# Kernel optimization log

Hardware: AMD Instinct MI355X
Metric: run time of the kernel (lower is better)

Reference implementation:

```python
import jax, jax.numpy as jnp
import numpy as np

N, IN, H, OUT, C = 1024, 64, 64, 64, 32
EPS = 1e-5   # SAKELayer.epsilon
INF = 1e5    # SAKELayer.inf


def _w(key, i, o, scale=1.0):
    return jax.random.normal(key, (i, o), jnp.float32) * (scale / np.sqrt(i))


def setup_inputs() -> dict:
    key = jax.random.key(0)
    ks = jax.random.split(key, 16)
    return dict(
        h=jax.random.normal(ks[0], (N, IN), jnp.float32),
        x=jax.random.normal(ks[1], (N, 3), jnp.float32),
        # edge model (ConcatenationFilter): Linear(2*IN+1,H), SiLU, Linear(H,H)
        ew1=_w(ks[2], 2 * IN + 1, H), eb1=jnp.zeros((H,), jnp.float32),
        ew2=_w(ks[3], H, H), eb2=jnp.zeros((H,), jnp.float32),
        # node_mlp: Linear(2H+IN,H), SiLU, Linear(H,OUT)
        nw1=_w(ks[4], 2 * H + IN, H), nb1=jnp.zeros((H,), jnp.float32),
        nw2=_w(ks[5], H, OUT), nb2=jnp.zeros((OUT,), jnp.float32),
        # coordinate_mlp: Linear(H,H), SiLU, Linear(H,1,bias=False) xavier gain 1e-3
        cw1=_w(ks[6], H, H), cb1=jnp.zeros((H,), jnp.float32),
        cw2=_w(ks[7], H, 1, scale=1e-3),
        # semantic_attention_mlp: Linear(H,1), LeakyReLU
        aw=_w(ks[8], H, 1), ab=jnp.zeros((1,), jnp.float32),
        # coefficients_mlp: Linear(H,H), SiLU, Linear(H,C)
        fw1=_w(ks[9], H, H), fb1=jnp.zeros((H,), jnp.float32),
        fw2=_w(ks[10], H, C), fb2=jnp.zeros((C,), jnp.float32),
        # post_norm_mlp: Linear(C,H), SiLU, Linear(H,H)
        pw1=_w(ks[11], C, H), pb1=jnp.zeros((H,), jnp.float32),
        pw2=_w(ks[12], H, H), pb2=jnp.zeros((H,), jnp.float32),
        log_gamma=jnp.array(0.0, jnp.float32),
    )


def reference(h, x, ew1, eb1, ew2, eb2, nw1, nb1, nw2, nb2, cw1, cb1, cw2,
              aw, ab, fw1, fb1, fw2, fb2, pw1, pb1, pw2, pb2, log_gamma):
    n, d_in = h.shape
    silu = jax.nn.silu
    eye = jnp.eye(n, dtype=h.dtype)[:, :, None]                    # [n,n,1]

    x_minus_xt = x[:, None, :] - x[None, :, :]                     # [n,n,3]
    norm = jnp.sqrt(jnp.sum(x_minus_xt ** 2, -1, keepdims=True) + EPS)  # [n,n,1]

    h_cat_ht = jnp.concatenate(
        [jnp.broadcast_to(h[:, None, :], (n, n, d_in)),
         jnp.broadcast_to(h[None, :, :], (n, n, d_in))], -1)       # [n,n,2*IN]

    # edge model: MLP over concat(features, distance)
    e_in = jnp.concatenate([h_cat_ht, norm], -1)                   # [n,n,2*IN+1]
    h_e = silu(e_in @ ew1 + eb1) @ ew2 + eb2                       # [n,n,H]

    # euclidean attention over neighbors j (diag masked by +INF distance)
    att_e = jax.nn.softmax(-(norm + INF * eye) * jnp.exp(log_gamma), axis=1)
    # semantic attention
    att_s = jax.nn.softmax(jax.nn.leaky_relu(h_e @ aw + ab) - INF * eye, axis=1)
    comb = att_e * att_s
    comb = comb / (jnp.sum(comb, axis=1, keepdims=True) + EPS)     # [n,n,1]
    h_e_att = h_e * comb                                           # [n,n,H]

    # spatial attention: equivariant coefficient combinations
    coeff = silu(h_e_att @ fw1 + fb1) @ fw2 + fb2                  # [n,n,C]
    dirs = x_minus_xt / (norm + 1.0)                               # [n,n,3]
    combos = jnp.einsum('ijc,ijd->icd', coeff, dirs) / n           # mean over j -> [n,C,3]
    h_comb = silu(jnp.sum(combos ** 2, -1) @ pw1 + pb1) @ pw2 + pb2  # [n,H]

    # node update
    h_agg = jnp.sum(h_e_att, axis=1)                               # [n,H]
    node_in = jnp.concatenate([h, h_agg, h_comb], -1)              # [n,2H+IN]
    h_out = h + (silu(node_in @ nw1 + nb1) @ nw2 + nb2)            # residual

    # equivariant coordinate update
    phi = silu(h_e @ cw1 + cb1) @ cw2                              # [n,n,1]
    x_out = x + jnp.mean(x_minus_xt * phi, axis=1)                 # [n,3]
    return h_out, x_out
```

## Files before the change

kernel.cpp:

```cpp
#include <hip/hip_runtime.h>
#include <hip/hip_bf16.h>

#define NN 1024
#define JT 128
#define LSTR 72
#define EPSV 1e-5f
#define BIGINF 1e5f

typedef __attribute__((ext_vector_type(8))) short short8;
typedef __attribute__((ext_vector_type(4))) short short4v;
typedef __attribute__((ext_vector_type(4))) float f32x4;

__device__ __forceinline__ float siluf(float v) {
    return v * __builtin_amdgcn_rcpf(1.0f + __expf(-v));
}
__device__ __forceinline__ float pnorm(float dx, float dy, float dz) {
    return sqrtf(dx * dx + dy * dy + dz * dz + EPSV);
}
__device__ __forceinline__ float wsum(float v) {
#pragma unroll
    for (int off = 32; off > 0; off >>= 1) v += __shfl_xor(v, off, 64);
    return v;
}
__device__ __forceinline__ float red16(float v) {
    v += __shfl_xor(v, 1, 64); v += __shfl_xor(v, 2, 64);
    v += __shfl_xor(v, 4, 64); v += __shfl_xor(v, 8, 64);
    return v;
}
__device__ __forceinline__ float redquad(float v) {
    v += __shfl_xor(v, 16, 64); v += __shfl_xor(v, 32, 64);
    return v;
}
__device__ __forceinline__ short f2bs(float v) {
    __hip_bfloat16 b = __float2bfloat16(v);
    return *reinterpret_cast<short*>(&b);
}
__device__ __forceinline__ short f2bt(float v) {
    return (short)(__float_as_uint(v) >> 16);
}

__global__ void kA(const float* __restrict__ h, const float* __restrict__ ew1,
                   const float* __restrict__ eb1, const float* __restrict__ ew2,
                   const float* __restrict__ cw1, const float* __restrict__ fw1,
                   const float* __restrict__ fw2, const float* __restrict__ aw,
                   const float* __restrict__ ab, const float* __restrict__ eb2,
                   float* __restrict__ HA, float* __restrict__ HB,
                   float* __restrict__ HBT, short* __restrict__ ew2T,
                   short* __restrict__ cw1T, short* __restrict__ fw1T,
                   short* __restrict__ fw2T, float* __restrict__ wsv,
                   float* __restrict__ svb) {
    const int b = blockIdx.x;
    const int o = threadIdx.x;
    if (b < NN) {
        const int i = b;
        float hv = h[i * 64 + o];
        float a = 0.f, bb = eb1[o];
#pragma unroll
        for (int k = 0; k < 64; k++) {
            float hk = __shfl(hv, k, 64);
            a += hk * ew1[k * 64 + o];
            bb += hk * ew1[(64 + k) * 64 + o];
        }
        HA[i * 64 + o] = a;
        HB[i * 64 + o] = bb;
        HBT[o * NN + i] = bb;
    } else if (b < NN + 64) {
        const int r = b - NN;
        ew2T[r * 64 + o] = f2bs(ew2[o * 64 + r]);
        cw1T[r * 64 + o] = f2bs(cw1[o * 64 + r]);
        fw1T[r * 64 + o] = f2bs(fw1[o * 64 + r]);
        if (r < 32) fw2T[r * 64 + o] = f2bs(fw2[o * 32 + r]);
    } else {
        float s = 0.f;
#pragma unroll
        for (int q = 0; q < 64; q++) s += ew2[o * 64 + q] * aw[q];
        wsv[o] = s;
        float e = wsum(eb2[o] * aw[o]);
        if (o == 0) svb[0] = e + ab[0];
    }
}

__global__ __launch_bounds__(256) void kBn(
    const float* __restrict__ x, const float* __restrict__ ew1,
    const float* __restrict__ HA, const float* __restrict__ HBT,
    const float* __restrict__ wsv, const float* __restrict__ svb,
    const float* __restrict__ lg, float* __restrict__ ls,
    float* __restrict__ rowm, float* __restrict__ rowd) {
    const int i = blockIdx.x;
    const int t = threadIdx.x;
    const float* HAi = HA + i * 64;
    const float* w1 = ew1 + 128 * 64;
    const float gamma = __expf(lg[0]);
    const float svb0 = svb[0];
    const float xi0 = x[i * 3 + 0], xi1 = x[i * 3 + 1], xi2 = x[i * 3 + 2];

    float4 xa = ((const float4*)x)[3 * t + 0];
    float4 xb = ((const float4*)x)[3 * t + 1];
    float4 xc = ((const float4*)x)[3 * t + 2];
    float nrm[4], le[4], lv[4];
    {
        float dx0 = xi0 - xa.x, dy0 = xi1 - xa.y, dz0 = xi2 - xa.z;
        float dx1 = xi0 - xa.w, dy1 = xi1 - xb.x, dz1 = xi2 - xb.y;
        float dx2 = xi0 - xb.z, dy2 = xi1 - xb.w, dz2 = xi2 - xc.x;
        float dx3 = xi0 - xc.y, dy3 = xi1 - xc.z, dz3 = xi2 - xc.w;
        nrm[0] = pnorm(dx0, dy0, dz0);
        nrm[1] = pnorm(dx1, dy1, dz1);
        nrm[2] = pnorm(dx2, dy2, dz2);
        nrm[3] = pnorm(dx3, dy3, dz3);
    }
    float d0 = 0.f, d1 = 0.f, d2 = 0.f, d3 = 0.f;
#pragma unroll 8
    for (int k = 0; k < 64; k++) {
        float4 hb = *(const float4*)&HBT[k * NN + 4 * t];
        float hk = HAi[k], w1k = w1[k], wv = wsv[k];
        d0 += siluf(hk + hb.x + nrm[0] * w1k) * wv;
        d1 += siluf(hk + hb.y + nrm[1] * w1k) * wv;
        d2 += siluf(hk + hb.z + nrm[2] * w1k) * wv;
        d3 += siluf(hk + hb.w + nrm[3] * w1k) * wv;
    }
    float me = -3.0e38f, ms = -3.0e38f;
    float4 svo;
    {
        float dd[4] = {d0, d1, d2, d3};
#pragma unroll
        for (int m = 0; m < 4; m++) {
            int j = 4 * t + m;
            float sv = dd[m] + svb0;
            sv = sv >= 0.f ? sv : 0.01f * sv;
            if (j == i) sv -= BIGINF;
            lv[m] = sv;
            le[m] = -(nrm[m] + (j == i ? BIGINF : 0.f)) * gamma;
            me = fmaxf(me, le[m]);
            ms = fmaxf(ms, lv[m]);
        }
        svo.x = lv[0]; svo.y = lv[1]; svo.z = lv[2]; svo.w = lv[3];
    }
    *(float4*)&ls[(size_t)i * NN + 4 * t] = svo;

    __shared__ float sm[4], ss[4], s1[4], s2[4], s3[4];
#pragma unroll
    for (int off = 32; off > 0; off >>= 1) {
        me = fmaxf(me, __shfl_xor(me, off, 64));
        ms = fmaxf(ms, __shfl_xor(ms, off, 64));
    }
    const int w = t >> 6;
    if ((t & 63) == 0) { sm[w] = me; ss[w] = ms; }
    __syncthreads();
    me = fmaxf(fmaxf(sm[0], sm[1]), fmaxf(sm[2], sm[3]));
    ms = fmaxf(fmaxf(ss[0], ss[1]), fmaxf(ss[2], ss[3]));
    float Se = 0.f, Ss = 0.f, Sq = 0.f;
#pragma unroll
    for (int m = 0; m < 4; m++) {
        float ee = __expf(le[m] - me);
        float es = __expf(lv[m] - ms);
        Se += ee; Ss += es; Sq += ee * es;
    }
    Se = wsum(Se); Ss = wsum(Ss); Sq = wsum(Sq);
    if ((t & 63) == 0) { s1[w] = Se; s2[w] = Ss; s3[w] = Sq; }
    __syncthreads();
    if (t == 0) {
        rowm[i] = me + ms;
        rowd[i] = (s3[0] + s3[1] + s3[2] + s3[3]) +
                  EPSV * (s1[0] + s1[1] + s1[2] + s1[3]) * (s2[0] + s2[1] + s2[2] + s2[3]);
    }
}

__device__ __forceinline__ void stageW(const short* __restrict__ g, short* s,
                                       int tid, int rows) {
    for (int c = tid; c < rows * 16; c += 512) {
        int r = c >> 4, q = c & 15;
        *(short4v*)&s[r * LSTR + q * 4] = *(const short4v*)&g[r * 64 + q * 4];
    }
}

__global__ __launch_bounds__(512) void kD(
    const float* __restrict__ x, const float* __restrict__ ew1,
    const float* __restrict__ eb2, const float* __restrict__ cb1,
    const float* __restrict__ cw2, const float* __restrict__ fb1,
    const float* __restrict__ fb2, const float* __restrict__ lg,
    const float* __restrict__ HA, const float* __restrict__ HB,
    const short* __restrict__ ew2T, const short* __restrict__ cw1T,
    const short* __restrict__ fw1T, const short* __restrict__ fw2T,
    const float* __restrict__ ls, const float* __restrict__ rowm,
    const float* __restrict__ rowd, float* __restrict__ hagg,
    float* __restrict__ combos, float* __restrict__ xupd) {
    __shared__ __align__(16) short sWe[64 * LSTR];
    __shared__ __align__(16) short sWc[64 * LSTR];
    __shared__ __align__(16) short sWf[64 * LSTR];
    __shared__ __align__(16) short sW2[32 * LSTR];
    __shared__ __align__(16) short sScr[8][16 * LSTR];
    __shared__ float sHag[64], sCombos[96], sXupd[3];

    const int tid = threadIdx.x;
    const int i = blockIdx.x;
    const int lane = tid & 63, w = tid >> 6;
    const int col = lane & 15, quad = lane >> 4;

    stageW(ew2T, sWe, tid, 64);
    stageW(cw1T, sWc, tid, 64);
    stageW(fw1T, sWf, tid, 64);
    stageW(fw2T, sW2, tid, 32);
    if (tid < 64) sHag[tid] = 0.f;
    else if (tid < 160) sCombos[tid - 64] = 0.f;
    else if (tid < 163) sXupd[tid - 160] = 0.f;

    short* scr = sScr[w];
    const float gamma = __expf(lg[0]);

    float w1r[2][8], har[2][8];
#pragma unroll
    for (int kb = 0; kb < 2; kb++)
#pragma unroll
        for (int t = 0; t < 8; t++) {
            w1r[kb][t] = ew1[128 * 64 + kb * 32 + quad * 8 + t];
            har[kb][t] = HA[i * 64 + kb * 32 + quad * 8 + t];
        }
    float eb[4], cbv[4], cwv[4], fbv[4];
#pragma unroll
    for (int nb = 0; nb < 4; nb++) {
        eb[nb] = eb2[nb * 16 + col];
        cbv[nb] = cb1[nb * 16 + col];
        cwv[nb] = cw2[nb * 16 + col];
        fbv[nb] = fb1[nb * 16 + col];
    }
    float fb2v[2] = {fb2[col], fb2[16 + col]};
    const float rm = rowm[i];
    const float invd = 1.0f / rowd[i];
    const float xi0 = x[i * 3 + 0], xi1 = x[i * 3 + 1], xi2 = x[i * 3 + 2];
    const float* lsi = ls + (size_t)i * NN;
    __syncthreads();

#pragma unroll 1
    for (int jt = 0; jt < 8; jt++) {
        const int jrow = jt * JT + w * 16 + col;
        float dxv = xi0 - x[jrow * 3 + 0];
        float dyv = xi1 - x[jrow * 3 + 1];
        float dzv = xi2 - x[jrow * 3 + 2];
        float nrmv = pnorm(dxv, dyv, dzv);
        float inv1 = __builtin_amdgcn_rcpf(nrmv + 1.0f);
        float fxv = dxv * inv1, fyv = dyv * inv1, fzv = dzv * inv1;
        float le = -(nrmv + (jrow == i ? BIGINF : 0.f)) * gamma;
        float combv = __expf(le + lsi[jrow] - rm) * invd;

        short8 afr[2];
#pragma unroll
        for (int kb = 0; kb < 2; kb++) {
            const float* hb = &HB[jrow * 64 + kb * 32 + quad * 8];
#pragma unroll
            for (int t = 0; t < 8; t++)
                afr[kb][t] = f2bt(siluf(har[kb][t] + hb[t] + nrmv * w1r[kb][t]));
        }
        f32x4 acc[4] = {{0.f, 0.f, 0.f, 0.f}, {0.f, 0.f, 0.f, 0.f},
                        {0.f, 0.f, 0.f, 0.f}, {0.f, 0.f, 0.f, 0.f}};
#pragma unroll
        for (int kb = 0; kb < 2; kb++) {
#pragma unroll
            for (int nb = 0; nb < 4; nb++) {
                short8 b = *(const short8*)&sWe[(nb * 16 + col) * LSTR + kb * 32 + quad * 8];
                acc[nb] = __builtin_amdgcn_mfma_f32_16x16x32_bf16(afr[kb], b, acc[nb], 0, 0, 0);
            }
        }
        {
            float hv[4][4], cmb[4];
#pragma unroll
            for (int reg = 0; reg < 4; reg++) cmb[reg] = __shfl(combv, quad * 4 + reg, 64);
#pragma unroll
            for (int reg = 0; reg < 4; reg++) {
#pragma unroll
                for (int nb = 0; nb < 4; nb++) {
                    hv[nb][reg] = acc[nb][reg] + eb[nb];
                    scr[(quad * 4 + reg) * LSTR + nb * 16 + col] = f2bt(hv[nb][reg]);
                }
            }
#pragma unroll
            for (int nb = 0; nb < 4; nb++) {
                float v = 0.f;
#pragma unroll
                for (int reg = 0; reg < 4; reg++) v += hv[nb][reg] * cmb[reg];
                v = redquad(v);
                if (quad == 0) atomicAdd(&sHag[nb * 16 + col], v);
            }
        }
        short8 a0 = *(const short8*)&scr[col * LSTR + quad * 8];
        short8 a1 = *(const short8*)&scr[col * LSTR + 32 + quad * 8];

        {
            f32x4 p[4] = {{0.f, 0.f, 0.f, 0.f}, {0.f, 0.f, 0.f, 0.f},
                          {0.f, 0.f, 0.f, 0.f}, {0.f, 0.f, 0.f, 0.f}};
#pragma unroll
            for (int nb = 0; nb < 4; nb++) {
                short8 b0 = *(const short8*)&sWc[(nb * 16 + col) * LSTR + quad * 8];
                short8 b1 = *(const short8*)&sWc[(nb * 16 + col) * LSTR + 32 + quad * 8];
                p[nb] = __builtin_amdgcn_mfma_f32_16x16x32_bf16(a0, b0, p[nb], 0, 0, 0);
                p[nb] = __builtin_amdgcn_mfma_f32_16x16x32_bf16(a1, b1, p[nb], 0, 0, 0);
            }
            float xa0 = 0.f, xa1 = 0.f, xa2 = 0.f;
#pragma unroll
            for (int reg = 0; reg < 4; reg++) {
                float ph = 0.f;
#pragma unroll
                for (int nb = 0; nb < 4; nb++) ph += siluf(p[nb][reg] + cbv[nb]) * cwv[nb];
                ph = red16(ph);
                float tdx = __shfl(dxv, quad * 4 + reg, 64);
                float tdy = __shfl(dyv, quad * 4 + reg, 64);
                float tdz = __shfl(dzv, quad * 4 + reg, 64);
                if (col == 0) { xa0 += ph * tdx; xa1 += ph * tdy; xa2 += ph * tdz; }
            }
            xa0 = wsum(xa0); xa1 = wsum(xa1); xa2 = wsum(xa2);
            if (lane == 0) {
                atomicAdd(&sXupd[0], xa0);
                atomicAdd(&sXupd[1], xa1);
                atomicAdd(&sXupd[2], xa2);
            }
        }

        {
            f32x4 vacc[4] = {{0.f, 0.f, 0.f, 0.f}, {0.f, 0.f, 0.f, 0.f},
                             {0.f, 0.f, 0.f, 0.f}, {0.f, 0.f, 0.f, 0.f}};
#pragma unroll
            for (int nb = 0; nb < 4; nb++) {
                short8 b0 = *(const short8*)&sWf[(nb * 16 + col) * LSTR + quad * 8];
                short8 b1 = *(const short8*)&sWf[(nb * 16 + col) * LSTR + 32 + quad * 8];
                vacc[nb] = __builtin_amdgcn_mfma_f32_16x16x32_bf16(a0, b0, vacc[nb], 0, 0, 0);
                vacc[nb] = __builtin_amdgcn_mfma_f32_16x16x32_bf16(a1, b1, vacc[nb], 0, 0, 0);
            }
            float cmb[4];
#pragma unroll
            for (int reg = 0; reg < 4; reg++) cmb[reg] = __shfl(combv, quad * 4 + reg, 64);
#pragma unroll
            for (int reg = 0; reg < 4; reg++) {
#pragma unroll
                for (int nb = 0; nb < 4; nb++)
                    scr[(quad * 4 + reg) * LSTR + nb * 16 + col] =
                        f2bt(siluf(cmb[reg] * vacc[nb][reg] + fbv[nb]));
            }
        }
        short8 wa0 = *(const short8*)&scr[col * LSTR + quad * 8];
        short8 wa1 = *(const short8*)&scr[col * LSTR + 32 + quad * 8];

        {
            f32x4 cacc[2] = {{0.f, 0.f, 0.f, 0.f}, {0.f, 0.f, 0.f, 0.f}};
#pragma unroll
            for (int nb = 0; nb < 2; nb++) {
                short8 b0 = *(const short8*)&sW2[(nb * 16 + col) * LSTR + quad * 8];
                short8 b1 = *(const short8*)&sW2[(nb * 16 + col) * LSTR + 32 + quad * 8];
                cacc[nb] = __builtin_amdgcn_mfma_f32_16x16x32_bf16(wa0, b0, cacc[nb], 0, 0, 0);
                cacc[nb] = __builtin_amdgcn_mfma_f32_16x16x32_bf16(wa1, b1, cacc[nb], 0, 0, 0);
            }
#pragma unroll
            for (int nb = 0; nb < 2; nb++) {
                float px = 0.f, py = 0.f, pz = 0.f;
#pragma unroll
                for (int reg = 0; reg < 4; reg++) {
                    float cf = cacc[nb][reg] + fb2v[nb];
                    float tfx = __shfl(fxv, quad * 4 + reg, 64);
                    float tfy = __shfl(fyv, quad * 4 + reg, 64);
                    float tfz = __shfl(fzv, quad * 4 + reg, 64);
                    px += cf * tfx; py += cf * tfy; pz += cf * tfz;
                }
                px = redquad(px); py = redquad(py); pz = redquad(pz);
                if (quad == 0) {
                    int c = nb * 16 + col;
                    atomicAdd(&sCombos[c * 3 + 0], px);
                    atomicAdd(&sCombos[c * 3 + 1], py);
                    atomicAdd(&sCombos[c * 3 + 2], pz);
                }
            }
        }
    }
    __syncthreads();
    if (tid < 64) hagg[i * 64 + tid] = sHag[tid];
    else if (tid < 160) combos[i * 96 + tid - 64] = sCombos[tid - 64];
    else if (tid < 163) xupd[i * 3 + tid - 160] = sXupd[tid - 160];
}

__global__ void kE(const float* __restrict__ h, const float* __restrict__ x,
                   const float* __restrict__ nw1, const float* __restrict__ nb1,
                   const float* __restrict__ nw2, const float* __restrict__ nb2,
                   const float* __restrict__ pw1, const float* __restrict__ pb1,
                   const float* __restrict__ pw2, const float* __restrict__ pb2,
                   const float* __restrict__ hagg, const float* __restrict__ combos,
                   const float* __restrict__ xupd, float* __restrict__ out) {
    const int i = blockIdx.x, o = threadIdx.x;
    const float invN = 1.0f / (float)NN;
    float r = 0.f;
    if (o < 32) {
        float v0 = combos[i * 96 + o * 3 + 0] * invN;
        float v1 = combos[i * 96 + o * 3 + 1] * invN;
        float v2 = combos[i * 96 + o * 3 + 2] * invN;
        r = v0 * v0 + v1 * v1 + v2 * v2;
    }
    float t1 = pb1[o];
#pragma unroll
    for (int k = 0; k < 32; k++) t1 += __shfl(r, k, 64) * pw1[k * 64 + o];
    t1 = siluf(t1);
    float hc = pb2[o];
#pragma unroll
    for (int k = 0; k < 64; k++) hc += __shfl(t1, k, 64) * pw2[k * 64 + o];
    float hi = h[i * 64 + o];
    float ha = hagg[i * 64 + o];
    float t2 = nb1[o];
#pragma unroll
    for (int k = 0; k < 64; k++) t2 += __shfl(hi, k, 64) * nw1[k * 64 + o];
#pragma unroll
    for (int k = 0; k < 64; k++) t2 += __shfl(ha, k, 64) * nw1[(64 + k) * 64 + o];
#pragma unroll
    for (int k = 0; k < 64; k++) t2 += __shfl(hc, k, 64) * nw1[(128 + k) * 64 + o];
    t2 = siluf(t2);
    float ho = hi + nb2[o];
#pragma unroll
    for (int k = 0; k < 64; k++) ho += __shfl(t2, k, 64) * nw2[k * 64 + o];
    out[i * 64 + o] = ho;
    if (o < 3)
        out[NN * 64 + i * 3 + o] = x[i * 3 + o] + xupd[i * 3 + o] * invN;
}

extern "C" void kernel_launch(void* const* d_in, const int* in_sizes, int n_in,
                              void* d_out, int out_size, void* d_ws, size_t ws_size,
                              hipStream_t stream) {
    (void)in_sizes; (void)n_in; (void)out_size; (void)ws_size;
    const float* h   = (const float*)d_in[0];
    const float* x   = (const float*)d_in[1];
    const float* ew1 = (const float*)d_in[2];
    const float* eb1 = (const float*)d_in[3];
    const float* ew2 = (const float*)d_in[4];
    const float* eb2 = (const float*)d_in[5];
    const float* nw1 = (const float*)d_in[6];
    const float* nb1 = (const float*)d_in[7];
    const float* nw2 = (const float*)d_in[8];
    const float* nb2 = (const float*)d_in[9];
    const float* cw1 = (const float*)d_in[10];
    const float* cb1 = (const float*)d_in[11];
    const float* cw2 = (const float*)d_in[12];
    const float* aw  = (const float*)d_in[13];
    const float* ab  = (const float*)d_in[14];
    const float* fw1 = (const float*)d_in[15];
    const float* fb1 = (const float*)d_in[16];
    const float* fw2 = (const float*)d_in[17];
    const float* fb2 = (const float*)d_in[18];
    const float* pw1 = (const float*)d_in[19];
    const float* pb1 = (const float*)d_in[20];
    const float* pw2 = (const float*)d_in[21];
    const float* pb2 = (const float*)d_in[22];
    const float* lg  = (const float*)d_in[23];
    float* out = (float*)d_out;

    float* W      = (float*)d_ws;
    float* ls     = W;
    float* HA     = ls + (size_t)NN * NN;
    float* HB     = HA + NN * 64;
    float* HBT    = HB + NN * 64;
    float* rowm   = HBT + NN * 64;
    float* rowd   = rowm + NN;
    float* hagg   = rowd + NN;
    float* combos = hagg + NN * 64;
    float* xupd   = combos + NN * 96;
    float* wsv    = xupd + NN * 3;
    float* svb    = wsv + 64;
    short* ew2T   = (short*)(svb + 4);
    short* cw1T   = ew2T + 64 * 64;
    short* fw1T   = cw1T + 64 * 64;
    short* fw2T   = fw1T + 64 * 64;

    kA<<<NN + 65, 64, 0, stream>>>(h, ew1, eb1, ew2, cw1, fw1, fw2, aw, ab, eb2,
                                   HA, HB, HBT, ew2T, cw1T, fw1T, fw2T, wsv, svb);
    kBn<<<NN, 256, 0, stream>>>(x, ew1, HA, HBT, wsv, svb, lg, ls, rowm, rowd);
    kD<<<NN, 512, 0, stream>>>(x, ew1, eb2, cb1, cw2, fb1, fb2, lg, HA, HB,
                               ew2T, cw1T, fw1T, fw2T, ls, rowm, rowd,
                               hagg, combos, xupd);
    kE<<<NN, 64, 0, stream>>>(h, x, nw1, nb1, nw2, nb2, pw1, pb1, pw2, pb2,
                              hagg, combos, xupd, out);
}
```

Measured before the change: 304.1 us.

## Process two 16-row j tiles per wave per iteration and read cw1 from global

Each wave now handles two interleaved 16-row edge tiles per loop iteration, halving the trip count and the number of reductions and shared atomics. Independent MFMA chains from the two tiles can interleave to hide latency. The coordinate-MLP weight cw1 is no longer staged in LDS and is read straight from global memory, which frees LDS for the doubled scratch buffers. The cost is much higher register pressure, possibly lowering occupancy, plus repeated global loads of cw1 that rely on cache hits.

Result: faster. 279.6 us, median of 2 (-8.1%).

```diff
diff --git a/kernel.cpp b/kernel.cpp
--- a/kernel.cpp
+++ b/kernel.cpp
@@ -2,7 +2,6 @@
 #include <hip/hip_bf16.h>
 
 #define NN 1024
-#define JT 128
 #define LSTR 72
 #define EPSV 1e-5f
 #define BIGINF 1e5f
@@ -185,10 +184,9 @@
     const float* __restrict__ rowd, float* __restrict__ hagg,
     float* __restrict__ combos, float* __restrict__ xupd) {
     __shared__ __align__(16) short sWe[64 * LSTR];
-    __shared__ __align__(16) short sWc[64 * LSTR];
     __shared__ __align__(16) short sWf[64 * LSTR];
     __shared__ __align__(16) short sW2[32 * LSTR];
-    __shared__ __align__(16) short sScr[8][16 * LSTR];
+    __shared__ __align__(16) short sScr[16][16 * LSTR];
     __shared__ float sHag[64], sCombos[96], sXupd[3];
 
     const int tid = threadIdx.x;
@@ -197,14 +195,14 @@
     const int col = lane & 15, quad = lane >> 4;
 
     stageW(ew2T, sWe, tid, 64);
-    stageW(cw1T, sWc, tid, 64);
     stageW(fw1T, sWf, tid, 64);
     stageW(fw2T, sW2, tid, 32);
     if (tid < 64) sHag[tid] = 0.f;
     else if (tid < 160) sCombos[tid - 64] = 0.f;
     else if (tid < 163) sXupd[tid - 160] = 0.f;
 
-    short* scr = sScr[w];
+    short* scr0 = sScr[2 * w];
+    short* scr1 = sScr[2 * w + 1];
     const float gamma = __expf(lg[0]);
 
     float w1r[2][8], har[2][8];
@@ -231,80 +229,102 @@
     __syncthreads();
 
 #pragma unroll 1
-    for (int jt = 0; jt < 8; jt++) {
-        const int jrow = jt * JT + w * 16 + col;
-        float dxv = xi0 - x[jrow * 3 + 0];
-        float dyv = xi1 - x[jrow * 3 + 1];
-        float dzv = xi2 - x[jrow * 3 + 2];
-        float nrmv = pnorm(dxv, dyv, dzv);
-        float inv1 = __builtin_amdgcn_rcpf(nrmv + 1.0f);
-        float fxv = dxv * inv1, fyv = dyv * inv1, fzv = dzv * inv1;
-        float le = -(nrmv + (jrow == i ? BIGINF : 0.f)) * gamma;
-        float combv = __expf(le + lsi[jrow] - rm) * invd;
-
-        short8 afr[2];
+    for (int jt = 0; jt < 4; jt++) {
+        const int r0 = jt * 256 + w * 16 + col;
+        const int r1 = r0 + 128;
+        float dx0 = xi0 - x[r0 * 3 + 0], dy0 = xi1 - x[r0 * 3 + 1], dz0 = xi2 - x[r0 * 3 + 2];
+        float dx1 = xi0 - x[r1 * 3 + 0], dy1 = xi1 - x[r1 * 3 + 1], dz1 = xi2 - x[r1 * 3 + 2];
+        float nr0 = pnorm(dx0, dy0, dz0), nr1 = pnorm(dx1, dy1, dz1);
+        float iv0 = __builtin_amdgcn_rcpf(nr0 + 1.0f), iv1 = __builtin_amdgcn_rcpf(nr1 + 1.0f);
+        float fx0 = dx0 * iv0, fy0 = dy0 * iv0, fz0 = dz0 * iv0;
+        float fx1 = dx1 * iv1, fy1 = dy1 * iv1, fz1 = dz1 * iv1;
+        float le0 = -(nr0 + (r0 == i ? BIGINF : 0.f)) * gamma;
+        float le1 = -(nr1 + (r1 == i ? BIGINF : 0.f)) * gamma;
+        float cb0 = __expf(le0 + lsi[r0] - rm) * invd;
+        float cb1f = __expf(le1 + lsi[r1] - rm) * invd;
+
+        short8 af0[2], af1[2];
 #pragma unroll
         for (int kb = 0; kb < 2; kb++) {
-            const float* hb = &HB[jrow * 64 + kb * 32 + quad * 8];
-#pragma unroll
-            for (int t = 0; t < 8; t++)
-                afr[kb][t] = f2bt(siluf(har[kb][t] + hb[t] + nrmv * w1r[kb][t]));
-        }
-        f32x4 acc[4] = {{0.f, 0.f, 0.f, 0.f}, {0.f, 0.f, 0.f, 0.f},
-                        {0.f, 0.f, 0.f, 0.f}, {0.f, 0.f, 0.f, 0.f}};
+            const float* hb0 = &HB[r0 * 64 + kb * 32 + quad * 8];
+            const float* hb1 = &HB[r1 * 64 + kb * 32 + quad * 8];
+#pragma unroll
+            for (int t = 0; t < 8; t++) {
+                af0[kb][t] = f2bt(siluf(har[kb][t] + hb0[t] + nr0 * w1r[kb][t]));
+                af1[kb][t] = f2bt(siluf(har[kb][t] + hb1[t] + nr1 * w1r[kb][t]));
+            }
+        }
+        f32x4 ac0[4] = {{0.f,0.f,0.f,0.f},{0.f,0.f,0.f,0.f},{0.f,0.f,0.f,0.f},{0.f,0.f,0.f,0.f}};
+        f32x4 ac1[4] = {{0.f,0.f,0.f,0.f},{0.f,0.f,0.f,0.f},{0.f,0.f,0.f,0.f},{0.f,0.f,0.f,0.f}};
 #pragma unroll
         for (int kb = 0; kb < 2; kb++) {
 #pragma unroll
             for (int nb = 0; nb < 4; nb++) {
                 short8 b = *(const short8*)&sWe[(nb * 16 + col) * LSTR + kb * 32 + quad * 8];
-                acc[nb] = __builtin_amdgcn_mfma_f32_16x16x32_bf16(afr[kb], b, acc[nb], 0, 0, 0);
+                ac0[nb] = __builtin_amdgcn_mfma_f32_16x16x32_bf16(af0[kb], b, ac0[nb], 0, 0, 0);
+                ac1[nb] = __builtin_amdgcn_mfma_f32_16x16x32_bf16(af1[kb], b, ac1[nb], 0, 0, 0);
             }
         }
         {
-            float hv[4][4], cmb[4];
-#pragma unroll
-            for (int reg = 0; reg < 4; reg++) cmb[reg] = __shfl(combv, quad * 4 + reg, 64);
+            float cm0[4], cm1[4];
 #pragma unroll
             for (int reg = 0; reg < 4; reg++) {
-#pragma unroll
-                for (int nb = 0; nb < 4; nb++) {
-                    hv[nb][reg] = acc[nb][reg] + eb[nb];
-                    scr[(quad * 4 + reg) * LSTR + nb * 16 + col] = f2bt(hv[nb][reg]);
-                }
+                cm0[reg] = __shfl(cb0, quad * 4 + reg, 64);
+                cm1[reg] = __shfl(cb1f, quad * 4 + reg, 64);
             }
 #pragma unroll
             for (int nb = 0; nb < 4; nb++) {
                 float v = 0.f;
 #pragma unroll
-                for (int reg = 0; reg < 4; reg++) v += hv[nb][reg] * cmb[reg];
+                for (int reg = 0; reg < 4; reg++) {
+                    float h0 = ac0[nb][reg] + eb[nb];
+                    float h1 = ac1[nb][reg] + eb[nb];
+                    scr0[(quad * 4 + reg) * LSTR + nb * 16 + col] = f2bt(h0);
+                    scr1[(quad * 4 + reg) * LSTR + nb * 16 + col] = f2bt(h1);
+                    v += h0 * cm0[reg] + h1 * cm1[reg];
+                }
                 v = redquad(v);
                 if (quad == 0) atomicAdd(&sHag[nb * 16 + col], v);
             }
         }
-        short8 a0 = *(const short8*)&scr[col * LSTR + quad * 8];
-        short8 a1 = *(const short8*)&scr[col * LSTR + 32 + quad * 8];
+        short8 a00 = *(const short8*)&scr0[col * LSTR + quad * 8];
+        short8 a01 = *(const short8*)&scr0[col * LSTR + 32 + quad * 8];
+        short8 a10 = *(const short8*)&scr1[col * LSTR + quad * 8];
+        short8 a11 = *(const short8*)&scr1[col * LSTR + 32 + quad * 8];
 
         {
-            f32x4 p[4] = {{0.f, 0.f, 0.f, 0.f}, {0.f, 0.f, 0.f, 0.f},
-                          {0.f, 0.f, 0.f, 0.f}, {0.f, 0.f, 0.f, 0.f}};
+            f32x4 p0[4] = {{0.f,0.f,0.f,0.f},{0.f,0.f,0.f,0.f},{0.f,0.f,0.f,0.f},{0.f,0.f,0.f,0.f}};
+            f32x4 p1[4] = {{0.f,0.f,0.f,0.f},{0.f,0.f,0.f,0.f},{0.f,0.f,0.f,0.f},{0.f,0.f,0.f,0.f}};
 #pragma unroll
             for (int nb = 0; nb < 4; nb++) {
-                short8 b0 = *(const short8*)&sWc[(nb * 16 + col) * LSTR + quad * 8];
-                short8 b1 = *(const short8*)&sWc[(nb * 16 + col) * LSTR + 32 + quad * 8];
-                p[nb] = __builtin_amdgcn_mfma_f32_16x16x32_bf16(a0, b0, p[nb], 0, 0, 0);
-                p[nb] = __builtin_amdgcn_mfma_f32_16x16x32_bf16(a1, b1, p[nb], 0, 0, 0);
+                short8 b0 = *(const short8*)&cw1T[(nb * 16 + col) * 64 + quad * 8];
+                short8 b1 = *(const short8*)&cw1T[(nb * 16 + col) * 64 + 32 + quad * 8];
+                p0[nb] = __builtin_amdgcn_mfma_f32_16x16x32_bf16(a00, b0, p0[nb], 0, 0, 0);
+                p0[nb] = __builtin_amdgcn_mfma_f32_16x16x32_bf16(a01, b1, p0[nb], 0, 0, 0);
+                p1[nb] = __builtin_amdgcn_mfma_f32_16x16x32_bf16(a10, b0, p1[nb], 0, 0, 0);
+                p1[nb] = __builtin_amdgcn_mfma_f32_16x16x32_bf16(a11, b1, p1[nb], 0, 0, 0);
             }
             float xa0 = 0.f, xa1 = 0.f, xa2 = 0.f;
 #pragma unroll
             for (int reg = 0; reg < 4; reg++) {
-                float ph = 0.f;
-#pragma unroll
-                for (int nb = 0; nb < 4; nb++) ph += siluf(p[nb][reg] + cbv[nb]) * cwv[nb];
-                ph = red16(ph);
-                float tdx = __shfl(dxv, quad * 4 + reg, 64);
-                float tdy = __shfl(dyv, quad * 4 + reg, 64);
-                float tdz = __shfl(dzv, quad * 4 + reg, 64);
-                if (col == 0) { xa0 += ph * tdx; xa1 += ph * tdy; xa2 += ph * tdz; }
+                float ph0 = 0.f, ph1 = 0.f;
+#pragma unroll
+                for (int nb = 0; nb < 4; nb++) {
+                    ph0 += siluf(p0[nb][reg] + cbv[nb]) * cwv[nb];
+                    ph1 += siluf(p1[nb][reg] + cbv[nb]) * cwv[nb];
+                }
+                ph0 = red16(ph0); ph1 = red16(ph1);
+                float t0x = __shfl(dx0, quad * 4 + reg, 64);
+                float t0y = __shfl(dy0, quad * 4 + reg, 64);
+                float t0z = __shfl(dz0, quad * 4 + reg, 64);
+                float t1x = __shfl(dx1, quad * 4 + reg, 64);
+                float t1y = __shfl(dy1, quad * 4 + reg, 64);
+                float t1z = __shfl(dz1, quad * 4 + reg, 64);
+                if (col == 0) {
+                    xa0 += ph0 * t0x + ph1 * t1x;
+                    xa1 += ph0 * t0y + ph1 * t1y;
+                    xa2 += ph0 * t0z + ph1 * t1z;
+                }
             }
             xa0 = wsum(xa0); xa1 = wsum(xa1); xa2 = wsum(xa2);
             if (lane == 0) {
@@ -315,48 +335,67 @@
         }
 
         {
-            f32x4 vacc[4] = {{0.f, 0.f, 0.f, 0.f}, {0.f, 0.f, 0.f, 0.f},
-                             {0.f, 0.f, 0.f, 0.f}, {0.f, 0.f, 0.f, 0.f}};
+            f32x4 v0[4] = {{0.f,0.f,0.f,0.f},{0.f,0.f,0.f,0.f},{0.f,0.f,0.f,0.f},{0.f,0.f,0.f,0.f}};
+            f32x4 v1[4] = {{0.f,0.f,0.f,0.f},{0.f,0.f,0.f,0.f},{0.f,0.f,0.f,0.f},{0.f,0.f,0.f,0.f}};
 #pragma unroll
             for (int nb = 0; nb < 4; nb++) {
                 short8 b0 = *(const short8*)&sWf[(nb * 16 + col) * LSTR + quad * 8];
                 short8 b1 = *(const short8*)&sWf[(nb * 16 + col) * LSTR + 32 + quad * 8];
-                vacc[nb] = __builtin_amdgcn_mfma_f32_16x16x32_bf16(a0, b0, vacc[nb], 0, 0, 0);
-                vacc[nb] = __builtin_amdgcn_mfma_f32_16x16x32_bf16(a1, b1, vacc[nb], 0, 0, 0);
-            }
-            float cmb[4];
-#pragma unroll
-            for (int reg = 0; reg < 4; reg++) cmb[reg] = __shfl(combv, quad * 4 + reg, 64);
+                v0[nb] = __builtin_amdgcn_mfma_f32_16x16x32_bf16(a00, b0, v0[nb], 0, 0, 0);
+                v0[nb] = __builtin_amdgcn_mfma_f32_16x16x32_bf16(a01, b1, v0[nb], 0, 0, 0);
+                v1[nb] = __builtin_amdgcn_mfma_f32_16x16x32_bf16(a10, b0, v1[nb], 0, 0, 0);
+                v1[nb] = __builtin_amdgcn_mfma_f32_16x16x32_bf16(a11, b1, v1[nb], 0, 0, 0);
+            }
+            float cm0[4], cm1[4];
 #pragma unroll
             for (int reg = 0; reg < 4; reg++) {
-#pragma unroll
-                for (int nb = 0; nb < 4; nb++)
-                    scr[(quad * 4 + reg) * LSTR + nb * 16 + col] =
-                        f2bt(siluf(cmb[reg] * vacc[nb][reg] + fbv[nb]));
-            }
-        }
-        short8 wa0 = *(const short8*)&scr[col * LSTR + quad * 8];
-        short8 wa1 = *(const short8*)&scr[col * LSTR + 32 + quad * 8];
+                cm0[reg] = __shfl(cb0, quad * 4 + reg, 64);
+                cm1[reg] = __shfl(cb1f, quad * 4 + reg, 64);
+            }
+#pragma unroll
+            for (int reg = 0; reg < 4; reg++) {
+#pragma unroll
+                for (int nb = 0; nb < 4; nb++) {
+                    scr0[(quad * 4 + reg) * LSTR + nb * 16 + col] =
+                        f2bt(siluf(cm0[reg] * v0[nb][reg] + fbv[nb]));
+                    scr1[(quad * 4 + reg) * LSTR + nb * 16 + col] =
+                        f2bt(siluf(cm1[reg] * v1[nb][reg] + fbv[nb]));
+                }
+            }
+        }
+        short8 wa00 = *(const short8*)&scr0[col * LSTR + quad * 8];
+        short8 wa01 = *(const short8*)&scr0[col * LSTR + 32 + quad * 8];
+        short8 wa10 = *(const short8*)&scr1[col * LSTR + quad * 8];
+        short8 wa11 = *(const short8*)&scr1[col * LSTR + 32 + quad * 8];
 
         {
-            f32x4 cacc[2] = {{0.f, 0.f, 0.f, 0.f}, {0.f, 0.f, 0.f, 0.f}};
+            f32x4 c0[2] = {{0.f,0.f,0.f,0.f},{0.f,0.f,0.f,0.f}};
+            f32x4 c1[2] = {{0.f,0.f,0.f,0.f},{0.f,0.f,0.f,0.f}};
 #pragma unroll
             for (int nb = 0; nb < 2; nb++) {
                 short8 b0 = *(const short8*)&sW2[(nb * 16 + col) * LSTR + quad * 8];
                 short8 b1 = *(const short8*)&sW2[(nb * 16 + col) * LSTR + 32 + quad * 8];
-                cacc[nb] = __builtin_amdgcn_mfma_f32_16x16x32_bf16(wa0, b0, cacc[nb], 0, 0, 0);
-                cacc[nb] = __builtin_amdgcn_mfma_f32_16x16x32_bf16(wa1, b1, cacc[nb], 0, 0, 0);
+                c0[nb] = __builtin_amdgcn_mfma_f32_16x16x32_bf16(wa00, b0, c0[nb], 0, 0, 0);
+                c0[nb] = __builtin_amdgcn_mfma_f32_16x16x32_bf16(wa01, b1, c0[nb], 0, 0, 0);
+                c1[nb] = __builtin_amdgcn_mfma_f32_16x16x32_bf16(wa10, b0, c1[nb], 0, 0, 0);
+                c1[nb] = __builtin_amdgcn_mfma_f32_16x16x32_bf16(wa11, b1, c1[nb], 0, 0, 0);
             }
 #pragma unroll
             for (int nb = 0; nb < 2; nb++) {
                 float px = 0.f, py = 0.f, pz = 0.f;
 #pragma unroll
                 for (int reg = 0; reg < 4; reg++) {
-                    float cf = cacc[nb][reg] + fb2v[nb];
-                    float tfx = __shfl(fxv, quad * 4 + reg, 64);
-                    float tfy = __shfl(fyv, quad * 4 + reg, 64);
-                    float tfz = __shfl(fzv, quad * 4 + reg, 64);
-                    px += cf * tfx; py += cf * tfy; pz += cf * tfz;
+                    float cf0 = c0[nb][reg] + fb2v[nb];
+                    float cf1 = c1[nb][reg] + fb2v[nb];
+                    float t0x = __shfl(fx0, quad * 4 + reg, 64);
+                    float t0y = __shfl(fy0, quad * 4 + reg, 64);
+                    float t0z = __shfl(fz0, quad * 4 + reg, 64);
+                    float t1x = __shfl(fx1, quad * 4 + reg, 64);
+                    float t1y = __shfl(fy1, quad * 4 + reg, 64);
+                    float t1z = __shfl(fz1, quad * 4 + reg, 64);
+                    px += cf0 * t0x + cf1 * t1x;
+                    py += cf0 * t0y + cf1 * t1y;
+                    pz += cf0 * t0z + cf1 * t1z;
                 }
                 px = redquad(px); py = redquad(py); pz = redquad(pz);
                 if (quad == 0) {
```
